# Kernel optimization log

Hardware: AMD Instinct MI355X
Metric: run time of the kernel (lower is better)

Reference implementation:

```python
import jax, jax.numpy as jnp
import numpy as np

EPS = 1e-7

def fake_quant(x, bits):
    """Per-tensor affine fake-quantization (dnn-gating TorchRoundToBits),
    matching torch.fake_quantize_per_tensor_affine with dynamic range."""
    fp_max = jax.lax.stop_gradient(jnp.max(x))
    fp_min = jax.lax.stop_gradient(jnp.min(x))
    qmax = float(2 ** bits - 1)
    qmin = 0.0
    scale = (fp_max - fp_min) / (qmax - qmin) + EPS
    zero_point = jnp.trunc(qmin - fp_min / scale)  # int() cast in torch truncates
    q = jnp.round(x / scale + zero_point)
    qc = jnp.clip(q, qmin, qmax)
    return (qc - zero_point) * scale

def conv2d(x, w, stride=1, padding=1):
    return jax.lax.conv_general_dilated(
        x, w,
        window_strides=(stride, stride),
        padding=[(padding, padding), (padding, padding)],
        dimension_numbers=('NCHW', 'OIHW', 'NCHW'))

def setup_inputs() -> dict:
    key = jax.random.key(0)
    k1, k2 = jax.random.split(key)
    x = jax.random.normal(k1, (32, 256, 56, 56), dtype=jnp.float32)
    # kaiming-like init for a 3x3 conv with 256 in-channels
    fan_in = 256 * 3 * 3
    weight = jax.random.normal(k2, (256, 256, 3, 3), dtype=jnp.float32) / np.sqrt(fan_in)
    return {"x": x, "weight": weight}

def reference(x, weight):
    WBITS, ABITS, PGABITS = 8, 8, 4
    TH = 0.99
    w_q = fake_quant(weight, WBITS)          # quantized weights (shared by both convs)
    msb_in = fake_quant(x, PGABITS)          # low-precision (MSB) input
    msb_out = conv2d(msb_in, w_q)            # [32,256,56,56] prediction pass
    lsb_in = fake_quant(x, ABITS) - msb_in   # residual (LSB) input
    lsb_out = conv2d(lsb_in, w_q)            # high-precision correction pass
    mask = (jax.nn.sigmoid(msb_out) > TH).astype(msb_out.dtype)
    return msb_out + mask * lsb_out
```

## Files before the change

### kernel.cpp

```cpp
#include <hip/hip_runtime.h>
#include <stdint.h>
#include <stddef.h>

typedef int v4i  __attribute__((ext_vector_type(4)));
typedef int v16i __attribute__((ext_vector_type(16)));

struct QParams {
  float s4, z4, s8, z8, sw, zw;
  float s4sw, s8sw;
  int dw;
};

__device__ __forceinline__ unsigned enc_f(float f) {
  unsigned u = __float_as_uint(f);
  return (u & 0x80000000u) ? ~u : (u | 0x80000000u);
}
__device__ __forceinline__ float dec_f(unsigned e) {
  unsigned u = (e & 0x80000000u) ? (e ^ 0x80000000u) : ~e;
  return __uint_as_float(u);
}

__global__ void k_init(unsigned* mm, unsigned* zp) {
  int t = threadIdx.x;
  if (t < 128) zp[t] = 0u;
  if (t == 0) { mm[0] = 0xFFFFFFFFu; mm[1] = 0u; mm[2] = 0xFFFFFFFFu; mm[3] = 0u; }
}

__global__ void k_minmax(const float4* __restrict__ p, int n4, unsigned* mm) {
  float lmin = 3.4e38f, lmax = -3.4e38f;
  for (int i = blockIdx.x * blockDim.x + threadIdx.x; i < n4; i += gridDim.x * blockDim.x) {
    float4 v = p[i];
    lmin = fminf(lmin, fminf(fminf(v.x, v.y), fminf(v.z, v.w)));
    lmax = fmaxf(lmax, fmaxf(fmaxf(v.x, v.y), fmaxf(v.z, v.w)));
  }
  for (int off = 32; off; off >>= 1) {
    lmin = fminf(lmin, __shfl_down(lmin, off, 64));
    lmax = fmaxf(lmax, __shfl_down(lmax, off, 64));
  }
  __shared__ float smin[4], smax[4];
  int w = threadIdx.x >> 6, lane = threadIdx.x & 63;
  if (lane == 0) { smin[w] = lmin; smax[w] = lmax; }
  __syncthreads();
  if (threadIdx.x == 0) {
    float a = fminf(fminf(smin[0], smin[1]), fminf(smin[2], smin[3]));
    float b = fmaxf(fmaxf(smax[0], smax[1]), fmaxf(smax[2], smax[3]));
    atomicMin(&mm[0], enc_f(a));
    atomicMax(&mm[1], enc_f(b));
  }
}

__global__ void k_params(const unsigned* mm, QParams* q) {
  float xmin = dec_f(mm[0]), xmax = dec_f(mm[1]);
  float wmin = dec_f(mm[2]), wmax = dec_f(mm[3]);
  float s4 = (xmax - xmin) / 15.0f + 1e-7f;
  float z4 = truncf(0.0f - xmin / s4);
  float s8 = (xmax - xmin) / 255.0f + 1e-7f;
  float z8 = truncf(0.0f - xmin / s8);
  float sw = (wmax - wmin) / 255.0f + 1e-7f;
  float zw = truncf(0.0f - wmin / sw);
  q->s4 = s4; q->z4 = z4; q->s8 = s8; q->z8 = z8; q->sw = sw; q->zw = zw;
  q->s4sw = s4 * sw; q->s8sw = s8 * sw;
  q->dw = 128 - (int)zw;
}

__global__ void k_quant_w(const float* __restrict__ w, const QParams* __restrict__ q,
                          char* __restrict__ Wc) {
  __shared__ char sm[2304];
  int b = blockIdx.x;
  int tid = threadIdx.x;
  float sw = q->sw, zw = q->zw;
  const float* src = w + (size_t)b * 2304;
#pragma unroll
  for (int j = 0; j < 9; ++j) {
    int o = j * 256 + tid;
    float qf = rintf(__fdiv_rn(src[o], sw) + zw);
    qf = fminf(fmaxf(qf, 0.0f), 255.0f);
    int c = o / 9, jj = o - c * 9;
    sm[jj * 256 + c] = (char)((int)qf - 128);
  }
  __syncthreads();
  if (tid < 64) {
#pragma unroll
    for (int j = 0; j < 9; ++j)
      *(unsigned*)(Wc + (size_t)j * 65536 + b * 256 + tid * 4) =
          *(const unsigned*)(sm + j * 256 + tid * 4);
  }
}

__device__ __forceinline__ void quant2(float v, float s4, float z4, float s8, float z8,
                                       char& o4, char& o8) {
  float q4 = rintf(__fdiv_rn(v, s4) + z4);
  q4 = fminf(fmaxf(q4, 0.0f), 15.0f);
  o4 = (char)(int)(q4 - z4);
  float q8 = rintf(__fdiv_rn(v, s8) + z8);
  q8 = fminf(fmaxf(q8, 0.0f), 255.0f);
  int t8 = (int)(q8 - z8);
  o8 = (char)max(-128, min(127, t8));
}

__global__ void k_quant_x(const float4* __restrict__ x4, const QParams* __restrict__ q,
                          char* __restrict__ A4, char* __restrict__ A8,
                          int* __restrict__ CS4, int* __restrict__ CS8) {
  __shared__ char sm4[56 * 260];
  __shared__ char sm8[56 * 260];
  __shared__ int cp4[56][4], cp8[56][4];
  int bx = blockIdx.x;
  int n = bx / 56, y = bx % 56;
  int tid = threadIdx.x;
  float s4 = q->s4, z4 = q->z4, s8 = q->s8, z8 = q->z8;
  const float4* xrow = x4 + (size_t)n * 200704 + y * 14;
#pragma unroll 2
  for (int it = 0; it < 14; ++it) {
    int idx = it * 256 + tid;
    int c = idx / 14, xq = idx - c * 14;
    float4 v = xrow[(size_t)c * 784 + xq];
    int b = (xq * 4) * 260 + c;
    char a0, b0; quant2(v.x, s4, z4, s8, z8, a0, b0);
    char a1, b1; quant2(v.y, s4, z4, s8, z8, a1, b1);
    char a2, b2; quant2(v.z, s4, z4, s8, z8, a2, b2);
    char a3, b3; quant2(v.w, s4, z4, s8, z8, a3, b3);
    sm4[b] = a0; sm4[b + 260] = a1; sm4[b + 520] = a2; sm4[b + 780] = a3;
    sm8[b] = b0; sm8[b + 260] = b1; sm8[b + 520] = b2; sm8[b + 780] = b3;
  }
  __syncthreads();
  if (tid < 224) {
    int xc = tid >> 2, qq = tid & 3;
    const unsigned* r4 = (const unsigned*)(sm4 + xc * 260 + qq * 64);
    const unsigned* r8 = (const unsigned*)(sm8 + xc * 260 + qq * 64);
    int a = 0, b = 0;
#pragma unroll
    for (int cw = 0; cw < 16; ++cw) {
      unsigned u = r4[cw], v = r8[cw];
      a += (int)(signed char)(u) + (int)(signed char)(u >> 8)
         + (int)(signed char)(u >> 16) + (int)(signed char)(u >> 24);
      b += (int)(signed char)(v) + (int)(signed char)(v >> 8)
         + (int)(signed char)(v >> 16) + (int)(signed char)(v >> 24);
    }
    cp4[xc][qq] = a; cp8[xc][qq] = b;
  }
  __syncthreads();
  int pixbase = n * 3136 + y * 56;
  if (tid < 56) {
    CS4[pixbase + tid] = cp4[tid][0] + cp4[tid][1] + cp4[tid][2] + cp4[tid][3];
    CS8[pixbase + tid] = cp8[tid][0] + cp8[tid][1] + cp8[tid][2] + cp8[tid][3];
  }
  unsigned* A4w = (unsigned*)A4;
  unsigned* A8w = (unsigned*)A8;
#pragma unroll 2
  for (int it = 0; it < 14; ++it) {
    int idx = it * 256 + tid;
    int xc = idx >> 6, wd = idx & 63;
    size_t o = (size_t)(pixbase + xc) * 64 + wd;
    A4w[o] = *(const unsigned*)(sm4 + xc * 260 + wd * 4);
    A8w[o] = *(const unsigned*)(sm8 + xc * 260 + wd * 4);
  }
}

__global__ void k_wsum(const int* __restrict__ CS4, const int* __restrict__ CS8,
                       int* __restrict__ S4, int* __restrict__ S8) {
  int p = blockIdx.x * 256 + threadIdx.x;
  if (p >= 100352) return;
  int rem = p % 3136;
  int y = rem / 56, xc = rem % 56;
  int a = 0, b = 0;
#pragma unroll
  for (int dy = -1; dy <= 1; ++dy) {
    if ((unsigned)(y + dy) >= 56u) continue;
#pragma unroll
    for (int dx = -1; dx <= 1; ++dx) {
      if ((unsigned)(xc + dx) >= 56u) continue;
      int qq = p + dy * 56 + dx;
      a += CS4[qq]; b += CS8[qq];
    }
  }
  S4[p] = a; S8[p] = b;
}

#define GLD16(gp, lp)                                                         \
  __builtin_amdgcn_global_load_lds((const __attribute__((address_space(1))) void*)(gp), \
                                   (__attribute__((address_space(3))) void*)(lp), 16, 0, 0)

__device__ __forceinline__ float pg_merge(int a4v, int a8v, float fs4, float fs8) {
  float msb = fs4 * (float)a4v;
  float c8  = fs8 * (float)a8v;
  float lsb = c8 - msb;
  float sig = 1.0f / (1.0f + expf(-msb));
  return msb + (sig > 0.99f ? lsb : 0.0f);
}

struct StagePtrs {
  const char* aBase0; const char* aBase1;
  const char* a8Base0; const char* a8Base1;
  const char* bBase0; const char* bBase1;
  const char* zp0;
  unsigned vm0, vm1;
};

__device__ __forceinline__ void issue_stage(int s, const StagePtrs& P,
                                            char* dA4, char* dA8, char* dB) {
  int win = s >> 2;
  int cs = (s & 3) << 6;
  int dy = win / 3 - 1;
  int dx = win - (dy + 1) * 3 - 1;
  int doff = (dy * 56 + dx) * 256 + cs;
  bool ok0 = (P.vm0 >> win) & 1;
  bool ok1 = (P.vm1 >> win) & 1;
  const char* g40 = ok0 ? P.aBase0 + doff : P.zp0;
  const char* g41 = ok1 ? P.aBase1 + doff : P.zp0;
  const char* g80 = ok0 ? P.a8Base0 + doff : P.zp0;
  const char* g81 = ok1 ? P.a8Base1 + doff : P.zp0;
  const char* gB0 = P.bBase0 + win * 65536 + cs;
  const char* gB1 = P.bBase1 + win * 65536 + cs;
  if (s >= 36) { gB0 = P.zp0; gB1 = P.zp0; }
  GLD16(g40, dA4);       GLD16(g41, dA4 + 1024);
  GLD16(g80, dA8);       GLD16(g81, dA8 + 1024);
  GLD16(gB0, dB);        GLD16(gB1, dB + 1024);
}

__global__ __launch_bounds__(256, 2) void k_conv(
    const char* __restrict__ A4, const char* __restrict__ A8,
    const char* __restrict__ Wc,
    const int* __restrict__ S4, const int* __restrict__ S8,
    const QParams* __restrict__ q, const char* __restrict__ zpage,
    float* __restrict__ out) {
  __shared__ char smA4[2][8192], smA8[2][8192], smB[2][8192];
  const size_t ASZ = 25690112;
  int tid = threadIdx.x;
  int w = tid >> 6, lane = tid & 63;
  int m0 = blockIdx.x * 128;
  int n0 = blockIdx.y * 128;
  int wm = w >> 1, wn = w & 1;

  int chunk = lane & 3;
  int r0 = (w << 5) + (lane >> 2);
  int r1 = r0 + 16;
  int cg0 = chunk ^ ((r0 >> 1) & 3);
  int cg1 = chunk ^ ((r1 >> 1) & 3);
  int p0 = m0 + r0, p1 = m0 + r1;
  int rem0 = p0 % 3136, rem1 = p1 % 3136;
  int y0 = rem0 / 56, x0 = rem0 % 56;
  int y1 = rem1 / 56, x1 = rem1 % 56;

  StagePtrs P;
  P.aBase0 = A4 + (size_t)p0 * 256 + cg0 * 16;
  P.aBase1 = A4 + (size_t)p1 * 256 + cg1 * 16;
  P.a8Base0 = P.aBase0 + ASZ;
  P.a8Base1 = P.aBase1 + ASZ;
  P.bBase0 = Wc + (n0 + r0) * 256 + cg0 * 16;
  P.bBase1 = Wc + (n0 + r1) * 256 + cg1 * 16;
  P.zp0 = zpage + chunk * 16;
  P.vm0 = 0; P.vm1 = 0;
#pragma unroll
  for (int win = 0; win < 9; ++win) {
    int dy = win / 3 - 1, dx = win % 3 - 1;
    P.vm0 |= (unsigned)(((unsigned)(y0 + dy) < 56u) & ((unsigned)(x0 + dx) < 56u)) << win;
    P.vm1 |= (unsigned)(((unsigned)(y1 + dy) < 56u) & ((unsigned)(x1 + dx) < 56u)) << win;
  }

  char* dA4 = &smA4[0][w << 11];
  char* dA8 = &smA8[0][w << 11];
  char* dB  = &smB[0][w << 11];
  const char* smA4f = &smA4[0][0];
  const char* smA8f = &smA8[0][0];
  const char* smBf  = &smB[0][0];

  v16i acc4[2][2] = {}, acc8[2][2] = {};
  int r31 = lane & 31, qh = lane >> 5;

  int offA[2][2], offB[2][2];
#pragma unroll
  for (int fm = 0; fm < 2; ++fm) {
    int row = wm * 64 + fm * 32 + r31;
    int swz = (row >> 1) & 3;
#pragma unroll
    for (int kc = 0; kc < 2; ++kc)
      offA[fm][kc] = row * 64 + (((kc * 2 + qh) ^ swz) << 4);
  }
#pragma unroll
  for (int fn = 0; fn < 2; ++fn) {
    int row = wn * 64 + fn * 32 + r31;
    int swz = (row >> 1) & 3;
#pragma unroll
    for (int kc = 0; kc < 2; ++kc)
      offB[fn][kc] = row * 64 + (((kc * 2 + qh) ^ swz) << 4);
  }

#define COMPUTE(BUF)                                                          \
  {                                                                           \
    _Pragma("unroll")                                                         \
    for (int kc = 0; kc < 2; ++kc) {                                          \
      v4i a4f[2], a8f[2], bf[2];                                              \
      _Pragma("unroll")                                                       \
      for (int fm = 0; fm < 2; ++fm) {                                        \
        a4f[fm] = *(const v4i*)(smA4f + (BUF) * 8192 + offA[fm][kc]);         \
        a8f[fm] = *(const v4i*)(smA8f + (BUF) * 8192 + offA[fm][kc]);         \
      }                                                                       \
      _Pragma("unroll")                                                       \
      for (int fn = 0; fn < 2; ++fn)                                          \
        bf[fn] = *(const v4i*)(smBf + (BUF) * 8192 + offB[fn][kc]);           \
      _Pragma("unroll")                                                       \
      for (int fm = 0; fm < 2; ++fm)                                          \
        _Pragma("unroll")                                                     \
        for (int fn = 0; fn < 2; ++fn) {                                      \
          acc4[fm][fn] = __builtin_amdgcn_mfma_i32_32x32x32_i8(a4f[fm], bf[fn], acc4[fm][fn], 0, 0, 0); \
          acc8[fm][fn] = __builtin_amdgcn_mfma_i32_32x32x32_i8(a8f[fm], bf[fn], acc8[fm][fn], 0, 0, 0); \
        }                                                                     \
    }                                                                         \
  }

  issue_stage(0, P, dA4, dA8, dB);
  for (int sp = 0; sp < 18; ++sp) {
    int s0 = sp * 2;
    issue_stage(s0 + 1, P, dA4 + 8192, dA8 + 8192, dB + 8192);
    asm volatile("s_waitcnt vmcnt(6)" ::: "memory");
    asm volatile("s_barrier" ::: "memory");
    COMPUTE(0);
    asm volatile("s_barrier" ::: "memory");
    issue_stage(s0 + 2, P, dA4, dA8, dB);
    asm volatile("s_waitcnt vmcnt(6)" ::: "memory");
    asm volatile("s_barrier" ::: "memory");
    COMPUTE(1);
    asm volatile("s_barrier" ::: "memory");
  }
  asm volatile("s_waitcnt vmcnt(0)" ::: "memory");
#undef COMPUTE

  float fs4 = q->s4sw, fs8 = q->s8sw;
  int dwv = q->dw;
#pragma unroll
  for (int fm = 0; fm < 2; ++fm)
#pragma unroll
    for (int fn = 0; fn < 2; ++fn) {
      int kout = n0 + wn * 64 + fn * 32 + r31;
      int pb = m0 + wm * 64 + fm * 32 + 4 * qh;
#pragma unroll
      for (int rg = 0; rg < 4; ++rg) {
        int pr = pb + 8 * rg;
        int4 sv4 = *(const int4*)(S4 + pr);
        int4 sv8 = *(const int4*)(S8 + pr);
        float4 res;
        res.x = pg_merge(acc4[fm][fn][rg * 4 + 0] + dwv * sv4.x,
                         acc8[fm][fn][rg * 4 + 0] + dwv * sv8.x, fs4, fs8);
        res.y = pg_merge(acc4[fm][fn][rg * 4 + 1] + dwv * sv4.y,
                         acc8[fm][fn][rg * 4 + 1] + dwv * sv8.y, fs4, fs8);
        res.z = pg_merge(acc4[fm][fn][rg * 4 + 2] + dwv * sv4.z,
                         acc8[fm][fn][rg * 4 + 2] + dwv * sv8.z, fs4, fs8);
        res.w = pg_merge(acc4[fm][fn][rg * 4 + 3] + dwv * sv4.w,
                         acc8[fm][fn][rg * 4 + 3] + dwv * sv8.w, fs4, fs8);
        int nimg = pr / 3136;
        int rem = pr - nimg * 3136;
        *(float4*)(out + (size_t)nimg * 802816 + (size_t)kout * 3136 + rem) = res;
      }
    }
}

extern "C" void kernel_launch(void* const* d_in, const int* in_sizes, int n_in,
                              void* d_out, int out_size, void* d_ws, size_t ws_size,
                              hipStream_t stream) {
  const float* x  = (const float*)d_in[0];
  const float* wt = (const float*)d_in[1];
  float* out = (float*)d_out;

  char* ws = (char*)d_ws;
  unsigned* mm = (unsigned*)ws;
  QParams* prm = (QParams*)(ws + 64);
  char* zpage = ws + 256;
  char* A4 = ws + 1024;
  const size_t ASZ = 25690112;
  char* A8 = A4 + ASZ;
  int* CS4 = (int*)(A8 + ASZ);
  int* CS8 = CS4 + 100352;
  int* S4  = CS8 + 100352;
  int* S8  = S4 + 100352;
  char* Wc = (char*)(S8 + 100352);

  k_init<<<1, 256, 0, stream>>>(mm, (unsigned*)zpage);
  k_minmax<<<1024, 256, 0, stream>>>((const float4*)x, 25690112 / 4, mm);
  k_minmax<<<64, 256, 0, stream>>>((const float4*)wt, 589824 / 4, mm + 2);
  k_params<<<1, 1, 0, stream>>>(mm, prm);
  k_quant_w<<<256, 256, 0, stream>>>(wt, prm, Wc);
  k_quant_x<<<1792, 256, 0, stream>>>((const float4*)x, prm, A4, A8, CS4, CS8);
  k_wsum<<<392, 256, 0, stream>>>(CS4, CS8, S4, S8);
  k_conv<<<dim3(784, 2), 256, 0, stream>>>(A4, A8, Wc, S4, S8, prm, zpage, out);
}
```

Baseline: 423.6 us.

## Triple-buffer conv LDS pipeline with single barrier, setprio, and XCD-aware block swizzle

Moves the implicit-GEMM conv main loop from double to triple LDS buffering, so each K-stage needs only one barrier and the next stage's loads are issued right after it, two stages ahead. MFMA compute is wrapped in s_setprio to favour issue from waves doing math. The 2D grid becomes a 1D grid remapped with a modulo-8 swizzle so neighbouring tiles and the two N-halves of each M-tile land on the same XCD to improve L2 reuse. LDS per block rises from 48KB to 72KB, which may limit occupancy relative to launch_bounds(256,2).

Result: no change. 422.5 us (-0.3%).

```diff
diff --git a/kernel.cpp b/kernel.cpp
--- a/kernel.cpp
+++ b/kernel.cpp
@@ -223,12 +223,15 @@
     const int* __restrict__ S4, const int* __restrict__ S8,
     const QParams* __restrict__ q, const char* __restrict__ zpage,
     float* __restrict__ out) {
-  __shared__ char smA4[2][8192], smA8[2][8192], smB[2][8192];
+  __shared__ char smA4[3][8192], smA8[3][8192], smB[3][8192];
   const size_t ASZ = 25690112;
   int tid = threadIdx.x;
   int w = tid >> 6, lane = tid & 63;
-  int m0 = blockIdx.x * 128;
-  int n0 = blockIdx.y * 128;
+
+  int bid = blockIdx.x;
+  int swz = (bid & 7) * 196 + (bid >> 3);
+  int m0 = (swz >> 1) * 128;
+  int n0 = (swz & 1) * 128;
   int wm = w >> 1, wn = w & 1;
 
   int chunk = lane & 3;
@@ -271,18 +274,18 @@
 #pragma unroll
   for (int fm = 0; fm < 2; ++fm) {
     int row = wm * 64 + fm * 32 + r31;
-    int swz = (row >> 1) & 3;
+    int swl = (row >> 1) & 3;
 #pragma unroll
     for (int kc = 0; kc < 2; ++kc)
-      offA[fm][kc] = row * 64 + (((kc * 2 + qh) ^ swz) << 4);
+      offA[fm][kc] = row * 64 + (((kc * 2 + qh) ^ swl) << 4);
   }
 #pragma unroll
   for (int fn = 0; fn < 2; ++fn) {
     int row = wn * 64 + fn * 32 + r31;
-    int swz = (row >> 1) & 3;
+    int swl = (row >> 1) & 3;
 #pragma unroll
     for (int kc = 0; kc < 2; ++kc)
-      offB[fn][kc] = row * 64 + (((kc * 2 + qh) ^ swz) << 4);
+      offB[fn][kc] = row * 64 + (((kc * 2 + qh) ^ swl) << 4);
   }
 
 #define COMPUTE(BUF)                                                          \
@@ -309,20 +312,28 @@
   }
 
   issue_stage(0, P, dA4, dA8, dB);
-  for (int sp = 0; sp < 18; ++sp) {
-    int s0 = sp * 2;
-    issue_stage(s0 + 1, P, dA4 + 8192, dA8 + 8192, dB + 8192);
-    asm volatile("s_waitcnt vmcnt(6)" ::: "memory");
-    asm volatile("s_barrier" ::: "memory");
-    COMPUTE(0);
-    asm volatile("s_barrier" ::: "memory");
-    issue_stage(s0 + 2, P, dA4, dA8, dB);
-    asm volatile("s_waitcnt vmcnt(6)" ::: "memory");
-    asm volatile("s_barrier" ::: "memory");
-    COMPUTE(1);
-    asm volatile("s_barrier" ::: "memory");
+  issue_stage(1, P, dA4 + 8192, dA8 + 8192, dB + 8192);
+
+#define PHASE(S, RB, WB)                                                      \
+  {                                                                           \
+    asm volatile("s_waitcnt vmcnt(6)" ::: "memory");                          \
+    asm volatile("s_barrier" ::: "memory");                                   \
+    issue_stage((S) + 2, P, dA4 + (WB) * 8192, dA8 + (WB) * 8192,             \
+                dB + (WB) * 8192);                                            \
+    __builtin_amdgcn_s_setprio(1);                                            \
+    COMPUTE(RB);                                                              \
+    __builtin_amdgcn_s_setprio(0);                                            \
+  }
+
+#pragma unroll 1
+  for (int sp = 0; sp < 12; ++sp) {
+    int s0 = sp * 3;
+    PHASE(s0,     0, 2);
+    PHASE(s0 + 1, 1, 0);
+    PHASE(s0 + 2, 2, 1);
   }
   asm volatile("s_waitcnt vmcnt(0)" ::: "memory");
+#undef PHASE
 #undef COMPUTE
 
   float fs4 = q->s4sw, fs8 = q->s8sw;
@@ -381,5 +392,5 @@
   k_quant_w<<<256, 256, 0, stream>>>(wt, prm, Wc);
   k_quant_x<<<1792, 256, 0, stream>>>((const float4*)x, prm, A4, A8, CS4, CS8);
   k_wsum<<<392, 256, 0, stream>>>(CS4, CS8, S4, S8);
-  k_conv<<<dim3(784, 2), 256, 0, stream>>>(A4, A8, Wc, S4, S8, prm, zpage, out);
-}
+  k_conv<<<dim3(1568), 256, 0, stream>>>(A4, A8, Wc, S4, S8, prm, zpage, out);
+}
```
